# Kernel optimization log

Hardware: AMD Instinct MI355X
Metric: run time of the kernel (lower is better)

The kernel has to match this reference:

```python
import jax, jax.numpy as jnp
import numpy as np

E = 1024
H = 16
HD = E // H  # head_dim = 64
N, T, S = 2, 2048, 2048
NEG = -1e9


def setup_inputs() -> dict:
    key = jax.random.key(0)
    ks = jax.random.split(key, 12)
    s = 0.02
    inp = {
        "query": jax.random.normal(ks[0], (N, T, E), jnp.float32),
        "key": jax.random.normal(ks[1], (N, S, E), jnp.float32),
        "value": jax.random.normal(ks[2], (N, S, E), jnp.float32),
        # causal mask: mask[i, j] == 0 means target i cannot attend to source j
        "attn_mask": jnp.tril(jnp.ones((T, S), jnp.float32)),
        "pad_mask": jnp.zeros((N, S), bool),
        "Wq": jax.random.normal(ks[3], (E, E), jnp.float32) * s,
        "bq": jnp.zeros((E,), jnp.float32),
        "Wk": jax.random.normal(ks[4], (E, E), jnp.float32) * s,
        "bk": jnp.zeros((E,), jnp.float32),
        "Wv": jax.random.normal(ks[5], (E, E), jnp.float32) * s,
        "bv": jnp.zeros((E,), jnp.float32),
        "Wp": jax.random.normal(ks[6], (E, E), jnp.float32) * s,
        "bp": jnp.zeros((E,), jnp.float32),
    }
    return inp


def reference(query, key, value, attn_mask, pad_mask, Wq, bq, Wk, bk, Wv, bv, Wp, bp):
    n, t, _ = query.shape
    _, srcl, _ = key.shape
    # Linear projections (torch Linear: x @ W.T + b), split into heads
    Q = (query @ Wq.T + bq).reshape(n, t, H, HD).transpose(0, 2, 1, 3)      # (N,H,T,HD)
    K = (key @ Wk.T + bk).reshape(n, srcl, H, HD).transpose(0, 2, 1, 3)     # (N,H,S,HD)
    V = (value @ Wv.T + bv).reshape(n, srcl, H, HD).transpose(0, 2, 1, 3)   # (N,H,S,HD)
    scores = jnp.einsum("nhtd,nhsd->nhts", Q, K) / jnp.sqrt(jnp.float32(HD))
    scores = jnp.where(pad_mask[:, None, None, :], NEG, scores)
    scores = jnp.where(attn_mask[None, None, :, :] == 0, NEG, scores)
    att = jax.nn.softmax(scores, axis=-1)  # dropout=0 (eval)
    Y = jnp.einsum("nhts,nhsd->nhtd", att, V)
    Y = Y.transpose(0, 2, 1, 3).reshape(n, t, E)
    return Y @ Wp.T + bp
```

## Files before the change

### kernel.cpp

```cpp
#include <hip/hip_runtime.h>
#include <hip/hip_bf16.h>

#define E_  1024
#define H_  16
#define HD_ 64
#define NB  2
#define T_  2048
#define S_  2048
#define KD  1024

typedef __attribute__((ext_vector_type(8))) short short8;
typedef __attribute__((ext_vector_type(4))) short short4v;
typedef __attribute__((ext_vector_type(4))) float floatx4;

static __device__ __forceinline__ unsigned short f2bf(float f) {
    unsigned int u = __float_as_uint(f);
    unsigned int r = (u + 0x7FFFu + ((u >> 16) & 1u)) >> 16;
    return (unsigned short)r;
}

static __device__ __forceinline__ floatx4 mfma16(short8 a, short8 b, floatx4 c) {
    return __builtin_amdgcn_mfma_f32_16x16x32_bf16(a, b, c, 0, 0, 0);
}

static __device__ __forceinline__ void gload_lds16(const void* g, void* l) {
    __builtin_amdgcn_global_load_lds(
        (const __attribute__((address_space(1))) unsigned int*)g,
        (__attribute__((address_space(3))) unsigned int*)l, 16, 0, 0);
}

__global__ __launch_bounds__(256) void conv_w_kernel(
    const float* __restrict__ wq, const float* __restrict__ wk,
    const float* __restrict__ wv, const float* __restrict__ wp,
    unsigned short* __restrict__ dst)
{
    int idx = blockIdx.x * 256 + threadIdx.x;
    for (int i4 = idx; i4 < (1 << 20); i4 += 131072) {
        int seg  = i4 >> 18;
        int off4 = i4 & ((1 << 18) - 1);
        const float* s = (seg == 0) ? wq : (seg == 1) ? wk : (seg == 2) ? wv : wp;
        float4 v = *(const float4*)&s[(size_t)off4 * 4];
        short4v b;
        b[0] = (short)f2bf(v.x); b[1] = (short)f2bf(v.y);
        b[2] = (short)f2bf(v.z); b[3] = (short)f2bf(v.w);
        *(short4v*)&dst[((size_t)seg << 20) + (size_t)off4 * 4] = b;
    }
}

__global__ __launch_bounds__(256) void proj_qkv_kernel(
    const float* __restrict__ q_in, const float* __restrict__ k_in, const float* __restrict__ v_in,
    const unsigned short* __restrict__ Wb,
    const float* __restrict__ bq, const float* __restrict__ bk, const float* __restrict__ bv,
    unsigned short* __restrict__ Qh, unsigned short* __restrict__ K2, unsigned short* __restrict__ V2)
{
    const int z = blockIdx.z;
    const float* X    = (z == 0) ? q_in : (z == 1) ? k_in : v_in;
    const unsigned short* W = Wb + ((size_t)z << 20);
    const float* bias = (z == 0) ? bq : (z == 1) ? bk : bv;
    unsigned short* dst = (z == 0) ? Qh : (z == 1) ? K2 : V2;

    __shared__ unsigned short As[128 * 32];
    __shared__ unsigned short Bs[128 * 32];

    const int tid  = threadIdx.x;
    const int lane = tid & 63;
    const int w    = tid >> 6;
    const int wm   = w >> 1, wn = w & 1;
    const int m0   = blockIdx.x * 128;
    const int e0   = blockIdx.y * 128;
    const int l15  = lane & 15, lg = lane >> 4;

    floatx4 acc[4][4];
#pragma unroll
    for (int mi = 0; mi < 4; ++mi)
#pragma unroll
        for (int ni = 0; ni < 4; ++ni)
            acc[mi][ni] = (floatx4){0.f, 0.f, 0.f, 0.f};

    const int brow_in_chunk = lane >> 2;
    const int bslot = (lane & 3) ^ (brow_in_chunk & 3);

    for (int kt = 0; kt < KD / 32; ++kt) {
        const int k0 = kt * 32;
#pragma unroll
        for (int j = 0; j < 2; ++j) {
            int c = w * 2 + j;
            int row = c * 16 + brow_in_chunk;
            gload_lds16(&W[(size_t)(e0 + row) * KD + k0 + bslot * 8], &Bs[c * 512]);
        }
#pragma unroll
        for (int i = 0; i < 4; ++i) {
            int fid = tid + i * 256;
            int row = fid >> 3, c4 = fid & 7;
            float4 va = *(const float4*)&X[(size_t)(m0 + row) * KD + k0 + c4 * 4];
            short4v sa;
            sa[0] = (short)f2bf(va.x); sa[1] = (short)f2bf(va.y);
            sa[2] = (short)f2bf(va.z); sa[3] = (short)f2bf(va.w);
            int slot = (c4 >> 1) ^ (row & 3);
            *(short4v*)&As[row * 32 + slot * 8 + (c4 & 1) * 4] = sa;
        }
        __syncthreads();

        short8 af[4], bf[4];
#pragma unroll
        for (int mi = 0; mi < 4; ++mi) {
            int r_ = wm * 64 + mi * 16 + l15;
            af[mi] = *(const short8*)&As[r_ * 32 + ((lg ^ (l15 & 3)) << 3)];
        }
#pragma unroll
        for (int ni = 0; ni < 4; ++ni) {
            int r_ = wn * 64 + ni * 16 + l15;
            bf[ni] = *(const short8*)&Bs[r_ * 32 + ((lg ^ (l15 & 3)) << 3)];
        }
#pragma unroll
        for (int mi = 0; mi < 4; ++mi)
#pragma unroll
            for (int ni = 0; ni < 4; ++ni)
                acc[mi][ni] = mfma16(af[mi], bf[ni], acc[mi][ni]);
        __syncthreads();
    }

#pragma unroll
    for (int mi = 0; mi < 4; ++mi) {
#pragma unroll
        for (int ni = 0; ni < 4; ++ni) {
            int e  = e0 + wn * 64 + ni * 16 + l15;
            float bb = bias[e];
            int hh = e >> 6, d = e & 63;
#pragma unroll
            for (int r = 0; r < 4; ++r) {
                int m = m0 + wm * 64 + mi * 16 + (lg << 2) + r;
                int nn = m >> 11, t = m & (T_ - 1);
                unsigned short val = f2bf(acc[mi][ni][r] + bb);
                size_t hb = (size_t)(nn * H_ + hh) * (T_ * HD_);
                if (z == 0) {
                    dst[hb + (size_t)t * HD_ + d] = val;
                } else if (z == 1) {
                    dst[hb + (t >> 6) * 4096 + (t & 63) * 64 +
                        (((d >> 3) ^ (t & 7)) << 3) + (d & 7)] = val;
                } else {
                    dst[hb + (t >> 6) * 4096 + d * 64 +
                        ((((t >> 3) & 7) ^ (d & 7)) << 3) + (t & 7)] = val;
                }
            }
        }
    }
}

__global__ __launch_bounds__(256) void flash_attn_kernel(
    const unsigned short* __restrict__ Qh, const unsigned short* __restrict__ K2,
    const unsigned short* __restrict__ V2, unsigned short* __restrict__ Y)
{
    const int linear = blockIdx.x;
    const int nid = (linear & 7) * 64 + (linear >> 3);
    const int pb = nid & 15, h = (nid >> 4) & 15, n = nid >> 8;

    const int tid = threadIdx.x, lane = tid & 63, w = tid >> 6;
    const int l15 = lane & 15, lg = lane >> 4;

    const unsigned short* Qp = Qh + (size_t)(n * H_ + h) * (T_ * HD_);
    const unsigned short* Kt = K2 + (size_t)(n * H_ + h) * (T_ * HD_);
    const unsigned short* Vt = V2 + (size_t)(n * H_ + h) * (T_ * HD_);

    __shared__ unsigned short Ks_l[4096];
    __shared__ unsigned short VT_l[4096];
    __shared__ unsigned short Ps[64][72];

    const int prow = w * 16 + lg * 4;
    const int arow = w * 16 + l15;
    const int sw7  = l15 & 7;

#pragma unroll
    for (int side = 0; side < 2; ++side) {
        const int qt = side ? (31 - pb) : pb;
        const int q0 = qt * 64;

        short8 qf[2];
#pragma unroll
        for (int ks = 0; ks < 2; ++ks)
            qf[ks] = *(const short8*)&Qp[(size_t)(q0 + arow) * HD_ + ks * 32 + lg * 8];

        floatx4 o[4];
        float lacc[4];
#pragma unroll
        for (int hi = 0; hi < 4; ++hi) o[hi] = (floatx4){0.f, 0.f, 0.f, 0.f};
#pragma unroll
        for (int r = 0; r < 4; ++r) lacc[r] = 0.f;

        for (int kb = 0; kb <= qt; ++kb) {
            __syncthreads();
            const unsigned short* Ksrc = Kt + kb * 4096;
            const unsigned short* Vsrc = Vt + kb * 4096;
#pragma unroll
            for (int j = 0; j < 2; ++j) {
                int c = w * 2 + j;
                gload_lds16(&Ksrc[c * 512 + lane * 8], &Ks_l[c * 512]);
                gload_lds16(&Vsrc[c * 512 + lane * 8], &VT_l[c * 512]);
            }
            __syncthreads();

            floatx4 sa[4];
#pragma unroll
            for (int ni = 0; ni < 4; ++ni) sa[ni] = (floatx4){0.f, 0.f, 0.f, 0.f};
            __builtin_amdgcn_s_setprio(1);
#pragma unroll
            for (int ks = 0; ks < 2; ++ks) {
                short8 kf[4];
#pragma unroll
                for (int ni = 0; ni < 4; ++ni)
                    kf[ni] = *(const short8*)
                        &Ks_l[(ni * 16 + l15) * 64 + (((ks * 4 + lg) ^ sw7) << 3)];
#pragma unroll
                for (int ni = 0; ni < 4; ++ni)
                    sa[ni] = mfma16(qf[ks], kf[ni], sa[ni]);
            }
            __builtin_amdgcn_s_setprio(0);

            const bool diag = (kb == qt);
            float pv[4][4];
#pragma unroll
            for (int ni = 0; ni < 4; ++ni)
#pragma unroll
                for (int r = 0; r < 4; ++r) {
                    float e = __expf(sa[ni][r] * 0.125f);
                    if (diag && (ni * 16 + l15 > prow + r)) e = 0.f;
                    pv[ni][r] = e;
                }
#pragma unroll
            for (int r = 0; r < 4; ++r)
                lacc[r] += (pv[0][r] + pv[1][r]) + (pv[2][r] + pv[3][r]);

#pragma unroll
            for (int ni = 0; ni < 4; ++ni)
#pragma unroll
                for (int r = 0; r < 4; ++r)
                    Ps[prow + r][(ni * 16 + l15) ^ (lg << 3)] = f2bf(pv[ni][r]);

            __builtin_amdgcn_s_setprio(1);
#pragma unroll
            for (int ks = 0; ks < 2; ++ks) {
                short8 pa = *(const short8*)
                    &Ps[arow][(ks * 32 + lg * 8) ^ ((l15 >> 2) << 3)];
                short8 vt[4];
#pragma unroll
                for (int hi = 0; hi < 4; ++hi)
                    vt[hi] = *(const short8*)
                        &VT_l[(hi * 16 + l15) * 64 + (((ks * 4 + lg) ^ sw7) << 3)];
#pragma unroll
                for (int hi = 0; hi < 4; ++hi)
                    o[hi] = mfma16(pa, vt[hi], o[hi]);
            }
            __builtin_amdgcn_s_setprio(0);
        }

        float linv[4];
#pragma unroll
        for (int r = 0; r < 4; ++r) {
            float l = lacc[r];
#pragma unroll
            for (int off = 1; off < 16; off <<= 1)
                l += __shfl_xor(l, off);
            linv[r] = 1.0f / l;
        }

#pragma unroll
        for (int hi = 0; hi < 4; ++hi) {
            int col = hi * 16 + l15;
#pragma unroll
            for (int r = 0; r < 4; ++r) {
                int t = q0 + prow + r;
                Y[((size_t)n * T_ + t) * E_ + h * HD_ + col] =
                    f2bf(o[hi][r] * linv[r]);
            }
        }
    }
}

__global__ __launch_bounds__(256) void proj_out_kernel(
    const unsigned short* __restrict__ Yb, const unsigned short* __restrict__ Wpb,
    const float* __restrict__ bp, float* __restrict__ out)
{
    __shared__ unsigned short As[128 * 32];
    __shared__ unsigned short Bs[128 * 32];

    const int tid  = threadIdx.x;
    const int lane = tid & 63;
    const int w    = tid >> 6;
    const int wm   = w >> 1, wn = w & 1;
    const int m0   = blockIdx.x * 128;
    const int e0   = blockIdx.y * 128;
    const int l15  = lane & 15, lg = lane >> 4;

    floatx4 acc[4][4];
#pragma unroll
    for (int mi = 0; mi < 4; ++mi)
#pragma unroll
        for (int ni = 0; ni < 4; ++ni)
            acc[mi][ni] = (floatx4){0.f, 0.f, 0.f, 0.f};

    const int rowc = lane >> 2;
    const int slot = (lane & 3) ^ (rowc & 3);

    for (int kt = 0; kt < E_ / 32; ++kt) {
        const int k0 = kt * 32;
#pragma unroll
        for (int j = 0; j < 2; ++j) {
            int c = w * 2 + j;
            int row = c * 16 + rowc;
            gload_lds16(&Yb[(size_t)(m0 + row) * E_ + k0 + slot * 8], &As[c * 512]);
            gload_lds16(&Wpb[(size_t)(e0 + row) * E_ + k0 + slot * 8], &Bs[c * 512]);
        }
        __syncthreads();

        short8 af[4], bfv[4];
#pragma unroll
        for (int mi = 0; mi < 4; ++mi) {
            int r_ = wm * 64 + mi * 16 + l15;
            af[mi] = *(const short8*)&As[r_ * 32 + ((lg ^ (l15 & 3)) << 3)];
        }
#pragma unroll
        for (int ni = 0; ni < 4; ++ni) {
            int r_ = wn * 64 + ni * 16 + l15;
            bfv[ni] = *(const short8*)&Bs[r_ * 32 + ((lg ^ (l15 & 3)) << 3)];
        }
#pragma unroll
        for (int mi = 0; mi < 4; ++mi)
#pragma unroll
            for (int ni = 0; ni < 4; ++ni)
                acc[mi][ni] = mfma16(af[mi], bfv[ni], acc[mi][ni]);
        __syncthreads();
    }

#pragma unroll
    for (int mi = 0; mi < 4; ++mi) {
#pragma unroll
        for (int ni = 0; ni < 4; ++ni) {
            int e = e0 + wn * 64 + ni * 16 + l15;
            float bb = bp[e];
#pragma unroll
            for (int r = 0; r < 4; ++r) {
                int m = m0 + wm * 64 + mi * 16 + (lg << 2) + r;
                out[(size_t)m * E_ + e] = acc[mi][ni][r] + bb;
            }
        }
    }
}

extern "C" void kernel_launch(void* const* d_in, const int* in_sizes, int n_in,
                              void* d_out, int out_size, void* d_ws, size_t ws_size,
                              hipStream_t stream) {
    const float* query = (const float*)d_in[0];
    const float* key_  = (const float*)d_in[1];
    const float* value = (const float*)d_in[2];
    const float* Wq = (const float*)d_in[5];
    const float* bq = (const float*)d_in[6];
    const float* Wk = (const float*)d_in[7];
    const float* bk = (const float*)d_in[8];
    const float* Wv = (const float*)d_in[9];
    const float* bv = (const float*)d_in[10];
    const float* Wp = (const float*)d_in[11];
    const float* bp = (const float*)d_in[12];
    float* out = (float*)d_out;

    const size_t P = (size_t)NB * H_ * T_ * HD_;
    unsigned short* Qh  = (unsigned short*)d_ws;
    unsigned short* K2  = Qh + P;
    unsigned short* V2  = K2 + P;
    unsigned short* Yb  = V2 + P;
    unsigned short* Wb  = Yb + P;
    unsigned short* Wpb = Wb + 3 * (1u << 20);

    conv_w_kernel<<<dim3(512), 256, 0, stream>>>(Wq, Wk, Wv, Wp, Wb);
    proj_qkv_kernel<<<dim3(32, 8, 3), 256, 0, stream>>>(
        query, key_, value, Wb, bq, bk, bv, Qh, K2, V2);
    flash_attn_kernel<<<dim3(512), 256, 0, stream>>>(Qh, K2, V2, Yb);
    proj_out_kernel<<<dim3(32, 8), 256, 0, stream>>>(Yb, Wpb, bp, out);
}
```

Baseline: 122.3 us.

## Pre-convert activations to bf16 and widen GEMM K-tile to 64

The weight-conversion kernel now also converts the query, key and value activations to bf16 in workspace. This lets the QKV projection stage both operands with direct global-to-LDS async loads instead of converting fp32 in registers. Both projection GEMMs now use a K-tile of 64 with an 8-way XOR swizzle, halving the number of barrier pairs per output tile. The cost is an extra pass over the fp32 inputs (a bf16 write plus re-read) and doubled shared memory per block. Yb now aliases the Xb buffer, which is safe only because Xb is dead by the time attention runs.

New measurement: 129.4 us. 1.06x slower.

```diff
diff --git a/kernel.cpp b/kernel.cpp
--- a/kernel.cpp
+++ b/kernel.cpp
@@ -29,38 +29,49 @@
         (__attribute__((address_space(3))) unsigned int*)l, 16, 0, 0);
 }
 
-__global__ __launch_bounds__(256) void conv_w_kernel(
+__global__ __launch_bounds__(256) void conv_all_kernel(
     const float* __restrict__ wq, const float* __restrict__ wk,
     const float* __restrict__ wv, const float* __restrict__ wp,
-    unsigned short* __restrict__ dst)
+    const float* __restrict__ qi, const float* __restrict__ ki,
+    const float* __restrict__ vi,
+    unsigned short* __restrict__ Wb, unsigned short* __restrict__ Xb)
 {
+    const int NW4 = 1 << 18;
+    const int NX4 = 1 << 20;
+    const int TOT = 4 * NW4 + 3 * NX4;
     int idx = blockIdx.x * 256 + threadIdx.x;
-    for (int i4 = idx; i4 < (1 << 20); i4 += 131072) {
-        int seg  = i4 >> 18;
-        int off4 = i4 & ((1 << 18) - 1);
-        const float* s = (seg == 0) ? wq : (seg == 1) ? wk : (seg == 2) ? wv : wp;
+    for (int i4 = idx; i4 < TOT; i4 += 262144) {
+        const float* s; unsigned short* d; int off4;
+        if (i4 < 4 * NW4) {
+            int seg = i4 >> 18; off4 = i4 & (NW4 - 1);
+            s = (seg == 0) ? wq : (seg == 1) ? wk : (seg == 2) ? wv : wp;
+            d = Wb + ((size_t)seg << 20);
+        } else {
+            int j = i4 - 4 * NW4; int seg = j >> 20; off4 = j & (NX4 - 1);
+            s = (seg == 0) ? qi : (seg == 1) ? ki : vi;
+            d = Xb + ((size_t)seg << 22);
+        }
         float4 v = *(const float4*)&s[(size_t)off4 * 4];
         short4v b;
         b[0] = (short)f2bf(v.x); b[1] = (short)f2bf(v.y);
         b[2] = (short)f2bf(v.z); b[3] = (short)f2bf(v.w);
-        *(short4v*)&dst[((size_t)seg << 20) + (size_t)off4 * 4] = b;
+        *(short4v*)&d[(size_t)off4 * 4] = b;
     }
 }
 
 __global__ __launch_bounds__(256) void proj_qkv_kernel(
-    const float* __restrict__ q_in, const float* __restrict__ k_in, const float* __restrict__ v_in,
-    const unsigned short* __restrict__ Wb,
+    const unsigned short* __restrict__ Xb, const unsigned short* __restrict__ Wb,
     const float* __restrict__ bq, const float* __restrict__ bk, const float* __restrict__ bv,
     unsigned short* __restrict__ Qh, unsigned short* __restrict__ K2, unsigned short* __restrict__ V2)
 {
     const int z = blockIdx.z;
-    const float* X    = (z == 0) ? q_in : (z == 1) ? k_in : v_in;
+    const unsigned short* X = Xb + ((size_t)z << 22);
     const unsigned short* W = Wb + ((size_t)z << 20);
     const float* bias = (z == 0) ? bq : (z == 1) ? bk : bv;
     unsigned short* dst = (z == 0) ? Qh : (z == 1) ? K2 : V2;
 
-    __shared__ unsigned short As[128 * 32];
-    __shared__ unsigned short Bs[128 * 32];
+    __shared__ unsigned short As[128 * 64];
+    __shared__ unsigned short Bs[128 * 64];
 
     const int tid  = threadIdx.x;
     const int lane = tid & 63;
@@ -77,46 +88,39 @@
         for (int ni = 0; ni < 4; ++ni)
             acc[mi][ni] = (floatx4){0.f, 0.f, 0.f, 0.f};
 
-    const int brow_in_chunk = lane >> 2;
-    const int bslot = (lane & 3) ^ (brow_in_chunk & 3);
-
-    for (int kt = 0; kt < KD / 32; ++kt) {
-        const int k0 = kt * 32;
-#pragma unroll
-        for (int j = 0; j < 2; ++j) {
-            int c = w * 2 + j;
-            int row = c * 16 + brow_in_chunk;
-            gload_lds16(&W[(size_t)(e0 + row) * KD + k0 + bslot * 8], &Bs[c * 512]);
-        }
-#pragma unroll
-        for (int i = 0; i < 4; ++i) {
-            int fid = tid + i * 256;
-            int row = fid >> 3, c4 = fid & 7;
-            float4 va = *(const float4*)&X[(size_t)(m0 + row) * KD + k0 + c4 * 4];
-            short4v sa;
-            sa[0] = (short)f2bf(va.x); sa[1] = (short)f2bf(va.y);
-            sa[2] = (short)f2bf(va.z); sa[3] = (short)f2bf(va.w);
-            int slot = (c4 >> 1) ^ (row & 3);
-            *(short4v*)&As[row * 32 + slot * 8 + (c4 & 1) * 4] = sa;
+    const int rc = lane >> 3;
+    const int sl = (lane & 7) ^ rc;
+
+    for (int kt = 0; kt < KD / 64; ++kt) {
+        const int k0 = kt * 64;
+#pragma unroll
+        for (int j = 0; j < 4; ++j) {
+            int c = w * 4 + j;
+            int row = c * 8 + rc;
+            gload_lds16(&X[(size_t)(m0 + row) * KD + k0 + sl * 8], &As[c * 512]);
+            gload_lds16(&W[(size_t)(e0 + row) * KD + k0 + sl * 8], &Bs[c * 512]);
         }
         __syncthreads();
 
-        short8 af[4], bf[4];
-#pragma unroll
-        for (int mi = 0; mi < 4; ++mi) {
-            int r_ = wm * 64 + mi * 16 + l15;
-            af[mi] = *(const short8*)&As[r_ * 32 + ((lg ^ (l15 & 3)) << 3)];
-        }
-#pragma unroll
-        for (int ni = 0; ni < 4; ++ni) {
-            int r_ = wn * 64 + ni * 16 + l15;
-            bf[ni] = *(const short8*)&Bs[r_ * 32 + ((lg ^ (l15 & 3)) << 3)];
-        }
-#pragma unroll
-        for (int mi = 0; mi < 4; ++mi)
-#pragma unroll
-            for (int ni = 0; ni < 4; ++ni)
-                acc[mi][ni] = mfma16(af[mi], bf[ni], acc[mi][ni]);
+#pragma unroll
+        for (int ks = 0; ks < 2; ++ks) {
+            short8 af[4], bf[4];
+#pragma unroll
+            for (int mi = 0; mi < 4; ++mi) {
+                int r_ = wm * 64 + mi * 16 + l15;
+                af[mi] = *(const short8*)&As[r_ * 64 + (((ks * 4 + lg) ^ (r_ & 7)) << 3)];
+            }
+#pragma unroll
+            for (int ni = 0; ni < 4; ++ni) {
+                int r_ = wn * 64 + ni * 16 + l15;
+                bf[ni] = *(const short8*)&Bs[r_ * 64 + (((ks * 4 + lg) ^ (r_ & 7)) << 3)];
+            }
+#pragma unroll
+            for (int mi = 0; mi < 4; ++mi)
+#pragma unroll
+                for (int ni = 0; ni < 4; ++ni)
+                    acc[mi][ni] = mfma16(af[mi], bf[ni], acc[mi][ni]);
+        }
         __syncthreads();
     }
 
@@ -280,8 +284,8 @@
     const unsigned short* __restrict__ Yb, const unsigned short* __restrict__ Wpb,
     const float* __restrict__ bp, float* __restrict__ out)
 {
-    __shared__ unsigned short As[128 * 32];
-    __shared__ unsigned short Bs[128 * 32];
+    __shared__ unsigned short As[128 * 64];
+    __shared__ unsigned short Bs[128 * 64];
 
     const int tid  = threadIdx.x;
     const int lane = tid & 63;
@@ -298,36 +302,39 @@
         for (int ni = 0; ni < 4; ++ni)
             acc[mi][ni] = (floatx4){0.f, 0.f, 0.f, 0.f};
 
-    const int rowc = lane >> 2;
-    const int slot = (lane & 3) ^ (rowc & 3);
-
-    for (int kt = 0; kt < E_ / 32; ++kt) {
-        const int k0 = kt * 32;
-#pragma unroll
-        for (int j = 0; j < 2; ++j) {
-            int c = w * 2 + j;
-            int row = c * 16 + rowc;
-            gload_lds16(&Yb[(size_t)(m0 + row) * E_ + k0 + slot * 8], &As[c * 512]);
-            gload_lds16(&Wpb[(size_t)(e0 + row) * E_ + k0 + slot * 8], &Bs[c * 512]);
+    const int rc = lane >> 3;
+    const int sl = (lane & 7) ^ rc;
+
+    for (int kt = 0; kt < E_ / 64; ++kt) {
+        const int k0 = kt * 64;
+#pragma unroll
+        for (int j = 0; j < 4; ++j) {
+            int c = w * 4 + j;
+            int row = c * 8 + rc;
+            gload_lds16(&Yb[(size_t)(m0 + row) * E_ + k0 + sl * 8], &As[c * 512]);
+            gload_lds16(&Wpb[(size_t)(e0 + row) * E_ + k0 + sl * 8], &Bs[c * 512]);
         }
         __syncthreads();
 
-        short8 af[4], bfv[4];
-#pragma unroll
-        for (int mi = 0; mi < 4; ++mi) {
-            int r_ = wm * 64 + mi * 16 + l15;
-            af[mi] = *(const short8*)&As[r_ * 32 + ((lg ^ (l15 & 3)) << 3)];
-        }
-#pragma unroll
-        for (int ni = 0; ni < 4; ++ni) {
-            int r_ = wn * 64 + ni * 16 + l15;
-            bfv[ni] = *(const short8*)&Bs[r_ * 32 + ((lg ^ (l15 & 3)) << 3)];
-        }
-#pragma unroll
-        for (int mi = 0; mi < 4; ++mi)
-#pragma unroll
-            for (int ni = 0; ni < 4; ++ni)
-                acc[mi][ni] = mfma16(af[mi], bfv[ni], acc[mi][ni]);
+#pragma unroll
+        for (int ks = 0; ks < 2; ++ks) {
+            short8 af[4], bf[4];
+#pragma unroll
+            for (int mi = 0; mi < 4; ++mi) {
+                int r_ = wm * 64 + mi * 16 + l15;
+                af[mi] = *(const short8*)&As[r_ * 64 + (((ks * 4 + lg) ^ (r_ & 7)) << 3)];
+            }
+#pragma unroll
+            for (int ni = 0; ni < 4; ++ni) {
+                int r_ = wn * 64 + ni * 16 + l15;
+                bf[ni] = *(const short8*)&Bs[r_ * 64 + (((ks * 4 + lg) ^ (r_ & 7)) << 3)];
+            }
+#pragma unroll
+            for (int mi = 0; mi < 4; ++mi)
+#pragma unroll
+                for (int ni = 0; ni < 4; ++ni)
+                    acc[mi][ni] = mfma16(af[mi], bf[ni], acc[mi][ni]);
+        }
         __syncthreads();
     }
 
@@ -366,13 +373,15 @@
     unsigned short* Qh  = (unsigned short*)d_ws;
     unsigned short* K2  = Qh + P;
     unsigned short* V2  = K2 + P;
-    unsigned short* Yb  = V2 + P;
-    unsigned short* Wb  = Yb + P;
-    unsigned short* Wpb = Wb + 3 * (1u << 20);
-
-    conv_w_kernel<<<dim3(512), 256, 0, stream>>>(Wq, Wk, Wv, Wp, Wb);
+    unsigned short* Wb  = V2 + P;
+    unsigned short* Xb  = Wb + (4u << 20);
+    unsigned short* Yb  = Xb;
+    unsigned short* Wpb = Wb + (3u << 20);
+
+    conv_all_kernel<<<dim3(1024), 256, 0, stream>>>(
+        Wq, Wk, Wv, Wp, query, key_, value, Wb, Xb);
     proj_qkv_kernel<<<dim3(32, 8, 3), 256, 0, stream>>>(
-        query, key_, value, Wb, bq, bk, bv, Qh, K2, V2);
+        Xb, Wb, bq, bk, bv, Qh, K2, V2);
     flash_attn_kernel<<<dim3(512), 256, 0, stream>>>(Qh, K2, V2, Yb);
     proj_out_kernel<<<dim3(32, 8), 256, 0, stream>>>(Yb, Wpb, bp, out);
 }
```
